# Optimization experiments

Hardware: AMD Instinct MI355X
Metric: run time of the kernel (lower is better)

## Reference

```python
import jax, jax.numpy as jnp
import numpy as np

jax.config.update("jax_enable_x64", True)

# config
B, S = 4, 4096
H_SIZE = 2048          # hidden_size
VOCAB = 128000         # engram_base_vocab_size
MAX_NGRAM = 3          # engram_max_ngram_size -> orders 2..3
PRIME = 500009         # engram_n_embed_per_ngram (same prime for every order)
N_HEAD = 4             # engram_n_head_per_ngram
E = 32                 # engram_embed_dim
KS = 4                 # short conv kernel size
NUM_ORDERS = MAX_NGRAM - 1
TOTAL_HEADS = NUM_ORDERS * N_HEAD
TOTAL_ROWS = PRIME * N_HEAD * NUM_ORDERS  # flat multi-head table rows


def setup_inputs() -> dict:
    key = jax.random.key(0)
    k_ids, k_h, k_tab, k_cw, k_hp, k_gp, k_op = jax.random.split(key, 7)
    input_ids = jax.random.randint(k_ids, (B, S), 0, VOCAB, dtype=jnp.int64)
    hidden_states = jax.random.normal(k_h, (B, S, H_SIZE), dtype=jnp.float32)
    # identity compressed-tokenizer mapping buffer
    mapping = jnp.arange(VOCAB, dtype=jnp.int64)
    # deterministic odd multipliers, seeded like _build_multipliers
    rng = np.random.default_rng(0 * 10007 + 0 * 1009)
    mults = rng.integers(1, 2 ** 31, size=(NUM_ORDERS, N_HEAD, MAX_NGRAM))
    multipliers = jnp.asarray(mults * 2 + 1, dtype=jnp.int64)
    table = 0.02 * jax.random.normal(k_tab, (TOTAL_ROWS, E), dtype=jnp.float32)
    conv_w = 0.1 * jax.random.normal(k_cw, (E, KS), dtype=jnp.float32)  # depthwise taps
    conv_b = jnp.zeros((E,), dtype=jnp.float32)
    Wh = 0.05 * jax.random.normal(k_hp, (E, TOTAL_HEADS * E), dtype=jnp.float32)
    Wg = 0.02 * jax.random.normal(k_gp, (E, H_SIZE), dtype=jnp.float32)
    Wo = 0.02 * jax.random.normal(k_op, (H_SIZE, E), dtype=jnp.float32)
    return {"input_ids": input_ids, "hidden_states": hidden_states,
            "mapping": mapping, "multipliers": multipliers, "table": table,
            "conv_w": conv_w, "conv_b": conv_b, "Wh": Wh, "Wg": Wg, "Wo": Wo}


def _hash_indices(compressed, multipliers):
    """XOR-mix n-gram hash indices -> [B, S, TOTAL_HEADS] int64."""
    all_idx = []
    offset = 0
    for oi, k in enumerate(range(2, MAX_NGRAM + 1)):
        # forward sliding window, clamped at last token (matches cat/expand trick)
        pos = jnp.minimum(jnp.arange(S)[:, None] + jnp.arange(k)[None, :], S - 1)  # [S,k]
        ng = compressed[:, pos]                                  # [B,S,k]
        m = multipliers[oi, :, :k]                               # [nh,k]
        prod = ng[:, :, None, :] * m[None, None, :, :]           # [B,S,nh,k]
        h = prod[..., 0]
        for p in range(1, k):
            h = h ^ prod[..., p]
        idx = h % PRIME + (offset + jnp.arange(N_HEAD, dtype=jnp.int64) * PRIME)
        all_idx.append(idx)
        offset += PRIME * N_HEAD
    return jnp.concatenate(all_idx, axis=-1)


def reference(input_ids, hidden_states, mapping, multipliers, table,
              conv_w, conv_b, Wh, Wg, Wo):
    compressed = mapping[input_ids]                              # [B,S]
    indices = _hash_indices(compressed, multipliers)             # [B,S,TOTAL_HEADS]
    emb = table[indices].reshape(B, S, TOTAL_HEADS * E)          # multi-head gather
    emb = emb @ Wh.T                                             # head_proj -> [B,S,E]
    # causal depthwise short conv (kernel KS, left pad KS-1)
    xp = jnp.pad(emb, ((0, 0), (KS - 1, 0), (0, 0)))
    emb = sum(xp[:, j:j + S, :] * conv_w[:, j] for j in range(KS)) + conv_b
    gate = jax.nn.sigmoid(hidden_states @ Wg.T)                  # [B,S,E]
    return (gate * emb) @ Wo.T                                   # [B,S,H_SIZE]
```

## Files before the change

### kernel.cpp

```cpp
#include <hip/hip_runtime.h>
#include <hip/hip_bf16.h>
#include <stdint.h>

#define HSZ 2048
#define PRIME 500009u
#define CHUNK 64
#define NCH 32
#define BUFB 8192
#define WGOFF 16384
#define IDXOFF 32768
#define A_OFF 0
#define E36_OFF 19008
#define EC_OFF 24192
#define GE_OFF 28416

typedef __attribute__((ext_vector_type(8))) short short8;
typedef __attribute__((ext_vector_type(4))) float f32x4;
typedef __attribute__((ext_vector_type(4))) unsigned uint4v;
typedef __attribute__((ext_vector_type(2))) unsigned uint2v;

#define MEMFENCE asm volatile("" ::: "memory")
#define BARRIER() do { MEMFENCE; __builtin_amdgcn_s_barrier(); MEMFENCE; } while (0)
#define WAIT_LGKM0 asm volatile("s_waitcnt lgkmcnt(0)" ::: "memory")
#define WAIT_VM(n) asm volatile("s_waitcnt vmcnt(" #n ")" ::: "memory")

__device__ __forceinline__ unsigned pk2(float x, float y) {
  __hip_bfloat162 h = __float22bfloat162_rn(make_float2(x, y));
  return *reinterpret_cast<unsigned*>(&h);
}
__device__ __forceinline__ short f2bf(float f) {
  __hip_bfloat16 h = __float2bfloat16(f);
  return *reinterpret_cast<short*>(&h);
}
__device__ __forceinline__ short8 pack8(float4 a, float4 b) {
  uint4v u = {pk2(a.x, a.y), pk2(a.z, a.w), pk2(b.x, b.y), pk2(b.z, b.w)};
  return __builtin_bit_cast(short8, u);
}
__device__ __forceinline__ short8 load8_bf(const float* __restrict__ p) {
  float4 a = *reinterpret_cast<const float4*>(p);
  float4 b = *reinterpret_cast<const float4*>(p + 4);
  return pack8(a, b);
}
__device__ __forceinline__ void gload_lds16(const float* g, void* l) {
  __builtin_amdgcn_global_load_lds(
      (const __attribute__((address_space(1))) void*)g,
      (__attribute__((address_space(3))) void*)l, 16, 0, 0);
}

__global__ __launch_bounds__(256, 4) void engram_fused(
    const int* __restrict__ ids, const int* __restrict__ mapping,
    const unsigned* __restrict__ mult, const float* __restrict__ table,
    const float* __restrict__ Wh, const float* __restrict__ hidden,
    const float* __restrict__ cw, const float* __restrict__ cb,
    const float* __restrict__ Wg, const float* __restrict__ Wo,
    float* __restrict__ out) {
  __shared__ __align__(16) char smem[IDXOFF + 1152];
  int* idx_lds = (int*)(smem + IDXOFF);
  short(*A_lds)[264] = (short(*)[264])(smem + A_OFF);
  float(*emb36)[36] = (float(*)[36])(smem + E36_OFF);
  float(*emb_c)[33] = (float(*)[33])(smem + EC_OFF);
  short(*ge_lds)[40] = (short(*)[40])(smem + GE_OFF);

  const int tid = threadIdx.x;
  const int wid = tid >> 6, lane = tid & 63;
  const int l16 = lane & 15, q = lane >> 4;
  const int t0 = blockIdx.x * 32;

  auto STAGE = [&](int buf, int kc) {
#pragma unroll
    for (int j = 0; j < 2; ++j) {
      int r0 = wid * 8 + j * 4;
      int r = r0 + (lane >> 4);
      unsigned c4 = (((unsigned)l16 * 16u) ^ (((unsigned)r & 7u) << 4)) >> 2;
      gload_lds16(hidden + (size_t)(t0 + r) * HSZ + kc * CHUNK + c4,
                  smem + buf * BUFB + r0 * 256);
    }
#pragma unroll
    for (int j = 0; j < 2; ++j) {
      int r0 = wid * 8 + j * 4;
      int r = r0 + (lane >> 4);
      unsigned c4 = (((unsigned)l16 * 16u) ^ (((unsigned)r & 7u) << 4)) >> 2;
      gload_lds16(Wg + (size_t)r * HSZ + kc * CHUNK + c4,
                  smem + WGOFF + buf * BUFB + r0 * 256);
    }
  };

#pragma unroll
  for (int p = 0; p < 2; ++p) {
    int hh = p * 256 + tid;
    if (hh < 288) {
      int slot = hh >> 3, head = hh & 7;
      int tg = t0 - 4 + slot;
      if (tg < 0) tg = 0;
      int b = tg >> 12, s = tg & 4095;
      const int* idb = ids + (b << 12);
      int s1 = s + 1 > 4095 ? 4095 : s + 1;
      int s2 = s + 2 > 4095 ? 4095 : s + 2;
      uint64_t c0 = (unsigned)mapping[idb[s]];
      uint64_t c1 = (unsigned)mapping[idb[s1]];
      uint64_t c2 = (unsigned)mapping[idb[s2]];
      int mb = head * 3;
      uint64_t h = (c0 * (uint64_t)mult[mb]) ^ (c1 * (uint64_t)mult[mb + 1]);
      if (head >= 4) h ^= c2 * (uint64_t)mult[mb + 2];
      idx_lds[hh] = (int)((unsigned)(h % PRIME) + (unsigned)head * PRIME);
    }
  }
  WAIT_LGKM0; BARRIER();

  float4 g[9];
#pragma unroll
  for (int p = 0; p < 9; ++p) {
    int task = p * 256 + tid;
    int r = task >> 3, c4 = (task & 7) * 4;
    int row = idx_lds[r];
    g[p] = *reinterpret_cast<const float4*>(table + (size_t)row * 32 + c4);
  }

  STAGE(0, 0);
  STAGE(1, 1);

  const int tt = wid >> 1, ee = wid & 1;
  const int R = tt * 16 + l16;
  const unsigned sw = ((unsigned)R & 7u) << 4;
  const int Rb = ee * 16 + l16;
  const unsigned swb = ((unsigned)Rb & 7u) << 4;
  const char* hrow = smem + R * 256;
  const char* wrow = smem + WGOFF + Rb * 256;
  f32x4 acc = {0.f, 0.f, 0.f, 0.f};
  const unsigned x0 = q * 32u;

  auto MLP_ITER = [&](int kc, bool stage_next) {
    const char* hb = hrow + (kc & 1) * BUFB;
    const char* wb = wrow + (kc & 1) * BUFB;
    float4 a0 = *reinterpret_cast<const float4*>(hb + (x0 ^ sw));
    float4 a1 = *reinterpret_cast<const float4*>(hb + ((x0 + 16) ^ sw));
    float4 a2 = *reinterpret_cast<const float4*>(hb + ((x0 + 128) ^ sw));
    float4 a3 = *reinterpret_cast<const float4*>(hb + ((x0 + 144) ^ sw));
    float4 b0 = *reinterpret_cast<const float4*>(wb + (x0 ^ swb));
    float4 b1 = *reinterpret_cast<const float4*>(wb + ((x0 + 16) ^ swb));
    float4 b2 = *reinterpret_cast<const float4*>(wb + ((x0 + 128) ^ swb));
    float4 b3 = *reinterpret_cast<const float4*>(wb + ((x0 + 144) ^ swb));
    short8 A0 = pack8(a0, a1), A1 = pack8(a2, a3);
    short8 B0 = pack8(b0, b1), B1 = pack8(b2, b3);
    WAIT_LGKM0;
    BARRIER();
    if (stage_next) STAGE(kc & 1, kc + 2);
    acc = __builtin_amdgcn_mfma_f32_16x16x32_bf16(A0, B0, acc, 0, 0, 0);
    acc = __builtin_amdgcn_mfma_f32_16x16x32_bf16(A1, B1, acc, 0, 0, 0);
  };

  for (int kc = 0; kc < NCH - 1; ++kc) {
    WAIT_VM(4);
    BARRIER();
    MLP_ITER(kc, kc < NCH - 2);
  }
  {
    WAIT_VM(0); BARRIER();
    MLP_ITER(NCH - 1, false);
  }

#pragma unroll
  for (int p = 0; p < 9; ++p) {
    int task = p * 256 + tid;
    int r = task >> 3, c4 = (task & 7) * 4;
    uint2v pk = {pk2(g[p].x, g[p].y), pk2(g[p].z, g[p].w)};
    *reinterpret_cast<uint2v*>(&A_lds[r >> 3][(r & 7) * 32 + c4]) = pk;
  }
  WAIT_LGKM0; BARRIER();

  for (int job = wid; job < 6; job += 4) {
    int jt = job >> 1;
    int base = (jt == 0) ? 0 : (jt == 1) ? 16 : 20;
    int e0 = (job & 1) * 16;
    f32x4 ac = {0.f, 0.f, 0.f, 0.f};
#pragma unroll
    for (int ks = 0; ks < 8; ++ks) {
      short8 wf = load8_bf(Wh + (size_t)(e0 + l16) * 256 + ks * 32 + q * 8);
      short8 a = *reinterpret_cast<const short8*>(&A_lds[base + l16][ks * 32 + q * 8]);
      ac = __builtin_amdgcn_mfma_f32_16x16x32_bf16(wf, a, ac, 0, 0, 0);
    }
    if (jt != 2 || l16 >= 12)
      *reinterpret_cast<f32x4*>(&emb36[base + l16][e0 + q * 4]) = ac;
  }
  WAIT_LGKM0; BARRIER();

#pragma unroll
  for (int it = 0; it < 4; ++it) {
    int ii = it * 256 + tid;
    int tl = ii >> 5, e = ii & 31;
    int s = (t0 & 4095) + tl;
    float a = cb[e];
#pragma unroll
    for (int j = 0; j < 4; ++j)
      if (s - 3 + j >= 0) a += cw[e * 4 + j] * emb36[tl + 1 + j][e];
    emb_c[tl][e] = a;
  }
  WAIT_LGKM0; BARRIER();

#pragma unroll
  for (int j = 0; j < 4; ++j) {
    int r = tt * 16 + q * 4 + j, c = ee * 16 + l16;
    float gt = 1.f / (1.f + __expf(-acc[j]));
    ge_lds[r][c] = f2bf(gt * emb_c[r][c]);
  }
  WAIT_LGKM0; BARRIER();

  short8 Af0 = *reinterpret_cast<const short8*>(&ge_lds[l16][q * 8]);
  short8 Af1 = *reinterpret_cast<const short8*>(&ge_lds[16 + l16][q * 8]);
  float* orow0 = out + (size_t)(t0 + l16) * HSZ;
  float* orow1 = out + (size_t)(t0 + 16 + l16) * HSZ;
  int hbase = wid * 512;
#pragma unroll 4
  for (int ht = 0; ht < 32; ++ht) {
    int h0 = hbase + ht * 16;
    short8 aw = load8_bf(Wo + (size_t)(h0 + l16) * 32 + q * 8);
    f32x4 z = {0.f, 0.f, 0.f, 0.f};
    f32x4 o0 = __builtin_amdgcn_mfma_f32_16x16x32_bf16(aw, Af0, z, 0, 0, 0);
    f32x4 o1 = __builtin_amdgcn_mfma_f32_16x16x32_bf16(aw, Af1, z, 0, 0, 0);
    *reinterpret_cast<f32x4*>(orow0 + h0 + q * 4) = o0;
    *reinterpret_cast<f32x4*>(orow1 + h0 + q * 4) = o1;
  }
}

extern "C" void kernel_launch(void* const* d_in, const int* in_sizes, int n_in,
                              void* d_out, int out_size, void* d_ws, size_t ws_size,
                              hipStream_t stream) {
  const int* ids = (const int*)d_in[0];
  const float* hidden = (const float*)d_in[1];
  const int* mapping = (const int*)d_in[2];
  const unsigned* mult = (const unsigned*)d_in[3];
  const float* table = (const float*)d_in[4];
  const float* cw = (const float*)d_in[5];
  const float* cb = (const float*)d_in[6];
  const float* Wh = (const float*)d_in[7];
  const float* Wg = (const float*)d_in[8];
  const float* Wo = (const float*)d_in[9];
  float* out = (float*)d_out;

  engram_fused<<<512, 256, 0, stream>>>(ids, mapping, mult, table, Wh, hidden,
                                        cw, cb, Wg, Wo, out);
}
```

Baseline: 76.40 us.

## Give each wave private LDS staging to drop per-iteration block barriers

Each wave now stages its own 16 rows of hidden and 16 rows of Wg into a private 16KB double-buffered LDS region, so the gate-MLP K loop needs only per-wave vmcnt waits and no workgroup barriers. This doubles the shared memory footprint to about 65KB, lowers launch bounds occupancy from 4 to 2 blocks, and loads Wg redundantly across the two waves that share an ee value. It also fuses the causal conv into the gate/multiply step, removing the emb_c buffer and one barrier.

Measured after the change: 74.93 us. No clear change (-1.9%).

```diff
diff --git a/kernel.cpp b/kernel.cpp
--- a/kernel.cpp
+++ b/kernel.cpp
@@ -6,13 +6,11 @@
 #define PRIME 500009u
 #define CHUNK 64
 #define NCH 32
-#define BUFB 8192
-#define WGOFF 16384
-#define IDXOFF 32768
+#define WAVE_REG 16384
+#define IDXOFF 65536
 #define A_OFF 0
 #define E36_OFF 19008
-#define EC_OFF 24192
-#define GE_OFF 28416
+#define GE_OFF 24192
 
 typedef __attribute__((ext_vector_type(8))) short short8;
 typedef __attribute__((ext_vector_type(4))) float f32x4;
@@ -47,7 +45,7 @@
       (__attribute__((address_space(3))) void*)l, 16, 0, 0);
 }
 
-__global__ __launch_bounds__(256, 4) void engram_fused(
+__global__ __launch_bounds__(256, 2) void engram_fused(
     const int* __restrict__ ids, const int* __restrict__ mapping,
     const unsigned* __restrict__ mult, const float* __restrict__ table,
     const float* __restrict__ Wh, const float* __restrict__ hidden,
@@ -58,30 +56,31 @@
   int* idx_lds = (int*)(smem + IDXOFF);
   short(*A_lds)[264] = (short(*)[264])(smem + A_OFF);
   float(*emb36)[36] = (float(*)[36])(smem + E36_OFF);
-  float(*emb_c)[33] = (float(*)[33])(smem + EC_OFF);
   short(*ge_lds)[40] = (short(*)[40])(smem + GE_OFF);
 
   const int tid = threadIdx.x;
   const int wid = tid >> 6, lane = tid & 63;
   const int l16 = lane & 15, q = lane >> 4;
   const int t0 = blockIdx.x * 32;
-
-  auto STAGE = [&](int buf, int kc) {
-#pragma unroll
-    for (int j = 0; j < 2; ++j) {
-      int r0 = wid * 8 + j * 4;
-      int r = r0 + (lane >> 4);
+  const int tt = wid >> 1, ee = wid & 1;
+
+  char* wavebase = smem + wid * WAVE_REG;
+
+  auto STAGE = [&](int kc) {
+    char* hb = wavebase + (kc & 1) * 8192;
+#pragma unroll
+    for (int j = 0; j < 4; ++j) {
+      int r = j * 4 + q;
       unsigned c4 = (((unsigned)l16 * 16u) ^ (((unsigned)r & 7u) << 4)) >> 2;
-      gload_lds16(hidden + (size_t)(t0 + r) * HSZ + kc * CHUNK + c4,
-                  smem + buf * BUFB + r0 * 256);
-    }
-#pragma unroll
-    for (int j = 0; j < 2; ++j) {
-      int r0 = wid * 8 + j * 4;
-      int r = r0 + (lane >> 4);
+      gload_lds16(hidden + (size_t)(t0 + tt * 16 + r) * HSZ + kc * CHUNK + c4,
+                  hb + j * 1024);
+    }
+#pragma unroll
+    for (int j = 0; j < 4; ++j) {
+      int r = j * 4 + q;
       unsigned c4 = (((unsigned)l16 * 16u) ^ (((unsigned)r & 7u) << 4)) >> 2;
-      gload_lds16(Wg + (size_t)r * HSZ + kc * CHUNK + c4,
-                  smem + WGOFF + buf * BUFB + r0 * 256);
+      gload_lds16(Wg + (size_t)(ee * 16 + r) * HSZ + kc * CHUNK + c4,
+                  hb + 4096 + j * 1024);
     }
   };
 
@@ -116,49 +115,41 @@
     g[p] = *reinterpret_cast<const float4*>(table + (size_t)row * 32 + c4);
   }
 
-  STAGE(0, 0);
-  STAGE(1, 1);
-
-  const int tt = wid >> 1, ee = wid & 1;
-  const int R = tt * 16 + l16;
-  const unsigned sw = ((unsigned)R & 7u) << 4;
-  const int Rb = ee * 16 + l16;
-  const unsigned swb = ((unsigned)Rb & 7u) << 4;
-  const char* hrow = smem + R * 256;
-  const char* wrow = smem + WGOFF + Rb * 256;
+  STAGE(0);
+  STAGE(1);
+
+  const unsigned swz = ((unsigned)l16 & 7u) << 4;
+  const char* hrow = wavebase + l16 * 256;
+  const char* wrow = wavebase + 4096 + l16 * 256;
+  const unsigned x0 = q * 32u;
   f32x4 acc = {0.f, 0.f, 0.f, 0.f};
-  const unsigned x0 = q * 32u;
 
   auto MLP_ITER = [&](int kc, bool stage_next) {
-    const char* hb = hrow + (kc & 1) * BUFB;
-    const char* wb = wrow + (kc & 1) * BUFB;
-    float4 a0 = *reinterpret_cast<const float4*>(hb + (x0 ^ sw));
-    float4 a1 = *reinterpret_cast<const float4*>(hb + ((x0 + 16) ^ sw));
-    float4 a2 = *reinterpret_cast<const float4*>(hb + ((x0 + 128) ^ sw));
-    float4 a3 = *reinterpret_cast<const float4*>(hb + ((x0 + 144) ^ sw));
-    float4 b0 = *reinterpret_cast<const float4*>(wb + (x0 ^ swb));
-    float4 b1 = *reinterpret_cast<const float4*>(wb + ((x0 + 16) ^ swb));
-    float4 b2 = *reinterpret_cast<const float4*>(wb + ((x0 + 128) ^ swb));
-    float4 b3 = *reinterpret_cast<const float4*>(wb + ((x0 + 144) ^ swb));
+    const char* hb = hrow + (kc & 1) * 8192;
+    const char* wb = wrow + (kc & 1) * 8192;
+    float4 a0 = *reinterpret_cast<const float4*>(hb + (x0 ^ swz));
+    float4 a1 = *reinterpret_cast<const float4*>(hb + ((x0 + 16) ^ swz));
+    float4 a2 = *reinterpret_cast<const float4*>(hb + ((x0 + 128) ^ swz));
+    float4 a3 = *reinterpret_cast<const float4*>(hb + ((x0 + 144) ^ swz));
+    float4 b0 = *reinterpret_cast<const float4*>(wb + (x0 ^ swz));
+    float4 b1 = *reinterpret_cast<const float4*>(wb + ((x0 + 16) ^ swz));
+    float4 b2 = *reinterpret_cast<const float4*>(wb + ((x0 + 128) ^ swz));
+    float4 b3 = *reinterpret_cast<const float4*>(wb + ((x0 + 144) ^ swz));
     short8 A0 = pack8(a0, a1), A1 = pack8(a2, a3);
     short8 B0 = pack8(b0, b1), B1 = pack8(b2, b3);
     WAIT_LGKM0;
-    BARRIER();
-    if (stage_next) STAGE(kc & 1, kc + 2);
+    if (stage_next) STAGE(kc + 2);
     acc = __builtin_amdgcn_mfma_f32_16x16x32_bf16(A0, B0, acc, 0, 0, 0);
     acc = __builtin_amdgcn_mfma_f32_16x16x32_bf16(A1, B1, acc, 0, 0, 0);
   };
 
   for (int kc = 0; kc < NCH - 1; ++kc) {
-    WAIT_VM(4);
-    BARRIER();
+    WAIT_VM(8);
     MLP_ITER(kc, kc < NCH - 2);
   }
-  {
-    WAIT_VM(0); BARRIER();
-    MLP_ITER(NCH - 1, false);
-  }
-
+  { WAIT_VM(0); MLP_ITER(NCH - 1, false); }
+
+  BARRIER();
 #pragma unroll
   for (int p = 0; p < 9; ++p) {
     int task = p * 256 + tid;
@@ -184,24 +175,21 @@
   }
   WAIT_LGKM0; BARRIER();
 
-#pragma unroll
-  for (int it = 0; it < 4; ++it) {
-    int ii = it * 256 + tid;
-    int tl = ii >> 5, e = ii & 31;
-    int s = (t0 & 4095) + tl;
-    float a = cb[e];
-#pragma unroll
-    for (int j = 0; j < 4; ++j)
-      if (s - 3 + j >= 0) a += cw[e * 4 + j] * emb36[tl + 1 + j][e];
-    emb_c[tl][e] = a;
-  }
-  WAIT_LGKM0; BARRIER();
-
-#pragma unroll
-  for (int j = 0; j < 4; ++j) {
-    int r = tt * 16 + q * 4 + j, c = ee * 16 + l16;
-    float gt = 1.f / (1.f + __expf(-acc[j]));
-    ge_lds[r][c] = f2bf(gt * emb_c[r][c]);
+  {
+    int c = ee * 16 + l16;
+    float4 cwv = *reinterpret_cast<const float4*>(cw + c * 4);
+    float cbv = cb[c];
+#pragma unroll
+    for (int j = 0; j < 4; ++j) {
+      int r = tt * 16 + q * 4 + j;
+      int s = (t0 & 4095) + r;
+      float v = cbv;
+#pragma unroll
+      for (int j2 = 0; j2 < 4; ++j2)
+        if (s - 3 + j2 >= 0) v += cwv[j2] * emb36[r + 1 + j2][c];
+      float gt = 1.f / (1.f + __expf(-acc[j]));
+      ge_lds[r][c] = f2bf(gt * v);
+    }
   }
   WAIT_LGKM0; BARRIER();
 
```
